# Kernel tuning notes

Measured on AMD Instinct MI355X. Metric: run time of the kernel, lower is better.

The kernel has to match this reference:

```python
import jax, jax.numpy as jnp
import numpy as np

E, H2, V = 128, 512, 50000  # embedding_size, hidden_size*2, output_size
H4 = 2 * H2


def _gru_cell(x, h, W_ih, W_hh, b_ih, b_hh):
    # PyTorch GRU cell: gates ordered (r, z, n)
    gi = x @ W_ih.T + b_ih
    gh = h @ W_hh.T + b_hh
    i_r, i_z, i_n = jnp.split(gi, 3, axis=-1)
    h_r, h_z, h_n = jnp.split(gh, 3, axis=-1)
    r = jax.nn.sigmoid(i_r + h_r)
    z = jax.nn.sigmoid(i_z + h_z)
    n = jnp.tanh(i_n + r * h_n)
    return (1.0 - z) * n + z * h


def setup_inputs() -> dict:
    key = jax.random.key(0)
    ks = jax.random.split(key, 24)
    B, T = 64, 400
    s = 0.02
    inp = {
        "input_ids": jax.random.randint(ks[0], (B, 1), 0, V),
        "pre_hidden": jax.random.normal(ks[1], (2, B, H2), jnp.float32),
        "encoder_outputs": jax.random.normal(ks[2], (B, T, H2), jnp.float32),
        "source_input": jax.random.randint(ks[3], (B, T), 0, V),
        "coverage_vector": jax.random.uniform(ks[4], (B, 1, T), jnp.float32),
        "emb_table": jax.random.normal(ks[5], (V, E), jnp.float32) * s,
        "W_ih0": jax.random.normal(ks[6], (3 * H2, E), jnp.float32) * s,
        "W_hh0": jax.random.normal(ks[7], (3 * H2, H2), jnp.float32) * s,
        "b_ih0": jnp.zeros((3 * H2,), jnp.float32),
        "b_hh0": jnp.zeros((3 * H2,), jnp.float32),
        "W_ih1": jax.random.normal(ks[8], (3 * H2, H2), jnp.float32) * s,
        "W_hh1": jax.random.normal(ks[9], (3 * H2, H2), jnp.float32) * s,
        "b_ih1": jnp.zeros((3 * H2,), jnp.float32),
        "b_hh1": jnp.zeros((3 * H2,), jnp.float32),
        "align_W": jax.random.normal(ks[10], (1, 3 * H2), jnp.float32) * s,
        "align_b": jnp.zeros((1,), jnp.float32),
        "cov_W": jax.random.normal(ks[11], (H2, 1), jnp.float32) * s,
        "cov_b": jnp.zeros((H2,), jnp.float32),
        "fc1_W": jax.random.normal(ks[12], (H4, H4), jnp.float32) * s,
        "fc1_b": jnp.zeros((H4,), jnp.float32),
        "fc2_W": jax.random.normal(ks[13], (V, H4), jnp.float32) * s,
        "fc2_b": jnp.zeros((V,), jnp.float32),
        "gen_W": jax.random.normal(ks[14], (1, H4 + E), jnp.float32) * s,
        "gen_b": jnp.zeros((1,), jnp.float32),
    }
    return inp


def reference(input_ids, pre_hidden, encoder_outputs, source_input, coverage_vector,
              emb_table, W_ih0, W_hh0, b_ih0, b_hh0, W_ih1, W_hh1, b_ih1, b_hh1,
              align_W, align_b, cov_W, cov_b, fc1_W, fc1_b, fc2_W, fc2_b, gen_W, gen_b):
    B, T = source_input.shape
    # embedding lookup (dropout omitted / eval mode)
    emb = emb_table[input_ids[:, 0]]                          # [B,E]
    # 2-layer GRU, single decode step
    h0 = _gru_cell(emb, pre_hidden[0], W_ih0, W_hh0, b_ih0, b_hh0)
    h1 = _gru_cell(h0, pre_hidden[1], W_ih1, W_hh1, b_ih1, b_hh1)
    current_hidden = jnp.stack([h0, h1], axis=0)              # [2,B,H2]
    s = h1                                                    # [B,H2]
    cov = coverage_vector[:, 0, :]                            # [B,T]
    # coverage projection: Linear(1 -> H2)
    cov_feat = cov[:, :, None] * cov_W[:, 0][None, None, :] + cov_b  # [B,T,H2]
    s_rep = jnp.broadcast_to(s[:, None, :], (B, T, s.shape[-1]))
    combine = jnp.concatenate([encoder_outputs, s_rep, cov_feat], axis=-1)  # [B,T,3*H2]
    scores = jnp.einsum('bti,i->bt', combine, align_W[0]) + align_b[0]
    attn = jax.nn.softmax(jnp.tanh(scores), axis=1)           # [B,T]
    # coverage loss: sum of elementwise min(attn, coverage)
    coverage_loss = jnp.sum(jnp.minimum(attn, cov))
    new_coverage = coverage_vector + attn[:, None, :]         # [B,1,T]
    context = jnp.einsum('bt,bth->bh', attn, encoder_outputs) # [B,H2]
    ni = jnp.tanh(jnp.concatenate([s, context], axis=-1) @ fc1_W.T + fc1_b)
    logits = ni @ fc2_W.T + fc2_b                             # [B,V]
    Pvocab = jax.nn.softmax(logits, axis=1)
    # vectorized copy distribution: scatter-add attention mass onto source token ids
    batch_idx = jnp.arange(B)[:, None]
    copy_prob = jnp.zeros((B, logits.shape[1]), logits.dtype).at[batch_idx, source_input].add(attn)
    gen_in = jnp.concatenate([context, s, emb], axis=-1)      # [B,H4+E]
    p_gen = jax.nn.sigmoid(gen_in @ gen_W.T + gen_b)          # [B,1]
    out = Pvocab * p_gen + copy_prob * (1.0 - p_gen)
    return (out, current_hidden, attn[:, None, :], copy_prob, new_coverage, coverage_loss)
```

## Files before the change

### kernel.cpp

```cpp
#include <hip/hip_runtime.h>
#include <hip/hip_bf16.h>
#include <cstddef>

#define BB 64
#define TT 400
#define EE 128
#define HH 512
#define H4 1024
#define VV 50000
#define NCH 8
#define LSTR 136

#define OFF_OUT     0
#define OFF_CURHID  (BB*VV)
#define OFF_ATTN    (OFF_CURHID + 2*BB*HH)
#define OFF_COPY    (OFF_ATTN + BB*TT)
#define OFF_NEWCOV  (OFF_COPY + BB*VV)
#define OFF_LOSS    (OFF_NEWCOV + BB*TT)

#define WS_S      0
#define WS_TS     (WS_S + BB*HH)
#define WS_ATTN   (WS_TS + BB*TT)
#define WS_NIB    (WS_ATTN + BB*TT)
#define WS_A1     (WS_NIB + BB*H4/2)
#define WS_AX0    (WS_A1 + BB*H4/2)
#define WS_AH0    (WS_AX0 + BB*EE/2)
#define WS_AH1    (WS_AH0 + BB*HH/2)
#define WS_AX1    (WS_AH1 + BB*HH/2)
#define WS_PGEN   (WS_AX1 + BB*HH/2)
#define WS_RM     (WS_PGEN + 64)
#define WS_RS     (WS_RM + 64)
#define WS_CTXP   (WS_RS + 64)
#define WS_LOGITS (WS_CTXP + BB*NCH*HH)

typedef __attribute__((ext_vector_type(8))) short short8v;
typedef __attribute__((ext_vector_type(4))) short short4v;
typedef __attribute__((ext_vector_type(4))) float f32x4;

__device__ __forceinline__ float wredsum(float v) {
#pragma unroll
  for (int o = 32; o > 0; o >>= 1) v += __shfl_down(v, o, 64);
  return v;
}
__device__ __forceinline__ float wredmax(float v) {
#pragma unroll
  for (int o = 32; o > 0; o >>= 1) v = fmaxf(v, __shfl_down(v, o, 64));
  return v;
}
__device__ __forceinline__ float dot4(float4 a, float4 b) {
  return a.x*b.x + a.y*b.y + a.z*b.z + a.w*b.w;
}
__device__ __forceinline__ float sigmoidf(float x) { return 1.f / (1.f + expf(-x)); }
__device__ __forceinline__ short bfh(float f) {
  union { __hip_bfloat16 h; short s; } u; u.h = __float2bfloat16(f); return u.s;
}
__device__ __forceinline__ float bf2f(short s) {
  union { unsigned int u; float f; } v; v.u = ((unsigned int)(unsigned short)s) << 16; return v.f;
}

__global__ void zero_prep_kernel(float* __restrict__ p, float* __restrict__ loss,
                                 float* __restrict__ rs,
                                 const float* __restrict__ embt, const int* __restrict__ ids,
                                 const float* __restrict__ preh,
                                 short* __restrict__ ax0, short* __restrict__ ah0,
                                 short* __restrict__ ah1) {
  int i = blockIdx.x * 256 + threadIdx.x;
  ((float4*)p)[i] = make_float4(0.f, 0.f, 0.f, 0.f);
  if (i == 0) loss[0] = 0.f;
  if (i < 64) rs[i] = 0.f;
  if (i < BB * EE) {
    int b = i >> 7, k = i & 127;
    ax0[i] = bfh(embt[(size_t)ids[b] * EE + k]);
  } else if (i < BB * EE + 2 * BB * HH) {
    int j = i - BB * EE;
    if (j < BB * HH) ah0[j] = bfh(preh[j]);
    else ah1[j - BB * HH] = bfh(preh[j]);
  }
}

template<int KX>
__global__ __launch_bounds__(384) void gru_mfma_kernel(
    const short* __restrict__ Ax, const short* __restrict__ Ah,
    const float* __restrict__ W_ih, const float* __restrict__ W_hh,
    const float* __restrict__ b_ih, const float* __restrict__ b_hh,
    const float* __restrict__ hprev,
    float* __restrict__ hout_f, float* __restrict__ hout_o,
    short* __restrict__ hout_b, int bstride) {
  __shared__ float P[2][3][16][16];
  const int w = threadIdx.x >> 6;
  const int lane = threadIdx.x & 63;
  const int r16 = lane & 15, kg = lane >> 4;
  const int j0 = (blockIdx.x & 31) * 16;
  const int bg = blockIdx.x >> 5;
  const int part = (w >= 3) ? 1 : 0;
  const int g = w - part * 3;
  const int K = part ? HH : KX;
  const float* Wm = part ? W_hh : W_ih;
  const short* Am = part ? Ah : Ax;

  f32x4 acc = {0.f, 0.f, 0.f, 0.f};
  const float* wp = Wm + (size_t)(g * HH + j0 + r16) * K + kg * 8;
  const short* ap = Am + (size_t)(bg * 16 + r16) * K + kg * 8;
#pragma unroll 4
  for (int k0 = 0; k0 < K; k0 += 32) {
    float4 w0 = *(const float4*)(wp + k0);
    float4 w1 = *(const float4*)(wp + k0 + 4);
    short8v a = *(const short8v*)(ap + k0);
    short8v bf;
    bf[0] = bfh(w0.x); bf[1] = bfh(w0.y); bf[2] = bfh(w0.z); bf[3] = bfh(w0.w);
    bf[4] = bfh(w1.x); bf[5] = bfh(w1.y); bf[6] = bfh(w1.z); bf[7] = bfh(w1.w);
    acc = __builtin_amdgcn_mfma_f32_16x16x32_bf16(a, bf, acc, 0, 0, 0);
  }
#pragma unroll
  for (int r = 0; r < 4; r++) P[part][g][kg * 4 + r][r16] = acc[r];
  __syncthreads();
  if (w == 0) {
    int col = j0 + r16;
    float bir = b_ih[col] + b_hh[col];
    float biz = b_ih[HH + col] + b_hh[HH + col];
    float bin = b_ih[2 * HH + col], bhn = b_hh[2 * HH + col];
#pragma unroll
    for (int r = 0; r < 4; r++) {
      int m = kg * 4 + r;
      int row = bg * 16 + m;
      float rv = sigmoidf(P[0][0][m][r16] + P[1][0][m][r16] + bir);
      float zv = sigmoidf(P[0][1][m][r16] + P[1][1][m][r16] + biz);
      float nv = tanhf(P[0][2][m][r16] + bin + rv * (P[1][2][m][r16] + bhn));
      float h = (1.f - zv) * nv + zv * hprev[(size_t)row * HH + col];
      hout_f[(size_t)row * HH + col] = h;
      hout_o[(size_t)row * HH + col] = h;
      hout_b[(size_t)row * bstride + col] = bfh(h);
    }
  }
}

__global__ void scores_kernel(const float* __restrict__ enc, const float* __restrict__ cov,
                              const float* __restrict__ aW, const float* __restrict__ ab,
                              const float* __restrict__ covW, const float* __restrict__ covb,
                              const float* __restrict__ s, float* __restrict__ ts) {
  int b = blockIdx.y;
  int wid = threadIdx.x >> 6, lane = threadIdx.x & 63;
  int t = blockIdx.x * 4 + wid;
  int i8 = lane * 8;
  const float* e = enc + ((size_t)b * TT + t) * HH + i8;
  float4 a0 = *(const float4*)&aW[i8],        a1 = *(const float4*)&aW[i8 + 4];
  float4 b0 = *(const float4*)&aW[HH + i8],   b1 = *(const float4*)&aW[HH + i8 + 4];
  float4 c0 = *(const float4*)&aW[2*HH + i8], c1 = *(const float4*)&aW[2*HH + i8 + 4];
  float4 s0 = *(const float4*)&s[(size_t)b * HH + i8], s1 = *(const float4*)&s[(size_t)b * HH + i8 + 4];
  float4 w0 = *(const float4*)&covW[i8],      w1 = *(const float4*)&covW[i8 + 4];
  float4 v0 = *(const float4*)&covb[i8],      v1 = *(const float4*)&covb[i8 + 4];
  float covbt = cov[b * TT + t];
  float p1 = dot4(*(const float4*)&e[0], a0) + dot4(*(const float4*)&e[4], a1)
           + dot4(s0, b0) + dot4(s1, b1)
           + dot4(v0, c0) + dot4(v1, c1);
  float p2 = dot4(w0, c0) + dot4(w1, c1);
  float d = wredsum(p1 + covbt * p2);
  if (lane == 0) ts[b * TT + t] = tanhf(d + ab[0]);
}

__global__ void attn_kernel(const float* __restrict__ ts, const float* __restrict__ cov,
                            const int* __restrict__ src,
                            float* __restrict__ wattn, float* __restrict__ dout,
                            float* __restrict__ outc) {
  int b = blockIdx.x, tid = threadIdx.x;
  int lane = tid & 63, wid = tid >> 6;
  __shared__ float sred[8];
  __shared__ float bval[2];
  float v = (tid < TT) ? ts[b * TT + tid] : -1e30f;
  float wm = wredmax(v);
  if (lane == 0) sred[wid] = wm;
  __syncthreads();
  if (wid == 0) {
    float r = (lane < 8) ? sred[lane] : -1e30f;
    r = wredmax(r);
    if (lane == 0) bval[0] = r;
  }
  __syncthreads();
  float m = bval[0];
  float e = (tid < TT) ? expf(v - m) : 0.f;
  float wsm = wredsum(e);
  __syncthreads();
  if (lane == 0) sred[wid] = wsm;
  __syncthreads();
  if (wid == 0) {
    float r = (lane < 8) ? sred[lane] : 0.f;
    r = wredsum(r);
    if (lane == 0) bval[1] = r;
  }
  __syncthreads();
  float denom = bval[1];
  float a = e / denom;
  float lp = 0.f;
  if (tid < TT) {
    wattn[b * TT + tid] = a;
    dout[OFF_ATTN + b * TT + tid] = a;
    float c = cov[b * TT + tid];
    dout[OFF_NEWCOV + b * TT + tid] = c + a;
    lp = fminf(a, c);
    atomicAdd(&outc[(size_t)b * VV + src[b * TT + tid]], a);
  }
  float wl = wredsum(lp);
  __syncthreads();
  if (lane == 0) sred[wid] = wl;
  __syncthreads();
  if (wid == 0) {
    float r = (lane < 8) ? sred[lane] : 0.f;
    r = wredsum(r);
    if (lane == 0) atomicAdd(&dout[OFF_LOSS], r);
  }
}

__global__ void ctx_part_kernel(const float* __restrict__ enc, const float* __restrict__ attn,
                                float* __restrict__ ctxp) {
  int b = blockIdx.x, c = blockIdx.y;
  int h = threadIdx.x;
  __shared__ float as[TT / NCH];
  if (h < TT / NCH) as[h] = attn[b * TT + c * (TT / NCH) + h];
  __syncthreads();
  const float* e = enc + ((size_t)b * TT + c * (TT / NCH)) * HH + h;
  float acc = 0.f;
#pragma unroll 10
  for (int t = 0; t < TT / NCH; t++) acc += as[t] * e[(size_t)t * HH];
  ctxp[((size_t)b * NCH + c) * HH + h] = acc;
}

__global__ void ctxred_pgen_kernel(const float* __restrict__ ctxp, const float* __restrict__ s,
                                   const float* __restrict__ embt, const int* __restrict__ ids,
                                   const float* __restrict__ gW, const float* __restrict__ gb,
                                   short* __restrict__ a1, float* __restrict__ pgen) {
  int b = blockIdx.x, tid = threadIdx.x;
  int lane = tid & 63, wid = tid >> 6;
  __shared__ float sred[8];
  float acc = 0.f;
#pragma unroll
  for (int c = 0; c < NCH; c++) acc += ctxp[((size_t)b * NCH + c) * HH + tid];
  a1[(size_t)b * H4 + HH + tid] = bfh(acc);
  float part = acc * gW[tid] + s[b * HH + tid] * gW[HH + tid];
  if (tid < EE) part += embt[(size_t)ids[b] * EE + tid] * gW[2 * HH + tid];
  float w = wredsum(part);
  if (lane == 0) sred[wid] = w;
  __syncthreads();
  if (wid == 0) {
    float r = (lane < 8) ? sred[lane] : 0.f;
    r = wredsum(r);
    if (lane == 0) pgen[b] = sigmoidf(r + gb[0]);
  }
}

__global__ __launch_bounds__(256) void fc1_kernel(const short* __restrict__ a1,
                                                  const float* __restrict__ W,
                                                  const float* __restrict__ bias,
                                                  short* __restrict__ nib) {
  __shared__ float part[4096];
  const int w = threadIdx.x >> 6;
  const int lane = threadIdx.x & 63;
  const int r16 = lane & 15, kg = lane >> 4;
  const int v0 = blockIdx.x * 16;
  const int kb = w * 256;

  f32x4 acc0 = {0.f,0.f,0.f,0.f}, acc1 = {0.f,0.f,0.f,0.f};
  f32x4 acc2 = {0.f,0.f,0.f,0.f}, acc3 = {0.f,0.f,0.f,0.f};
  const float* wp = W + (size_t)(v0 + r16) * H4 + kb + kg * 8;
  const short* ap = a1 + (size_t)r16 * H4 + kb + kg * 8;
#pragma unroll 4
  for (int k0 = 0; k0 < 256; k0 += 32) {
    float4 w0 = *(const float4*)(wp + k0);
    float4 w1 = *(const float4*)(wp + k0 + 4);
    short8v a0 = *(const short8v*)(ap + k0);
    short8v a1v = *(const short8v*)(ap + 16 * H4 + k0);
    short8v a2 = *(const short8v*)(ap + 32 * H4 + k0);
    short8v a3 = *(const short8v*)(ap + 48 * H4 + k0);
    short8v bf;
    bf[0] = bfh(w0.x); bf[1] = bfh(w0.y); bf[2] = bfh(w0.z); bf[3] = bfh(w0.w);
    bf[4] = bfh(w1.x); bf[5] = bfh(w1.y); bf[6] = bfh(w1.z); bf[7] = bfh(w1.w);
    acc0 = __builtin_amdgcn_mfma_f32_16x16x32_bf16(a0, bf, acc0, 0, 0, 0);
    acc1 = __builtin_amdgcn_mfma_f32_16x16x32_bf16(a1v, bf, acc1, 0, 0, 0);
    acc2 = __builtin_amdgcn_mfma_f32_16x16x32_bf16(a2, bf, acc2, 0, 0, 0);
    acc3 = __builtin_amdgcn_mfma_f32_16x16x32_bf16(a3, bf, acc3, 0, 0, 0);
  }
  float* pb = part + w * 1024;
#pragma unroll
  for (int r = 0; r < 4; r++) {
    pb[(kg * 4 + r) * 16 + r16]      = acc0[r];
    pb[(16 + kg * 4 + r) * 16 + r16] = acc1[r];
    pb[(32 + kg * 4 + r) * 16 + r16] = acc2[r];
    pb[(48 + kg * 4 + r) * 16 + r16] = acc3[r];
  }
  __syncthreads();
  int idx = threadIdx.x * 4;
  int m = idx >> 4, c0 = idx & 15;
  f32x4 s0 = *(const f32x4*)(part + idx);
  f32x4 s1 = *(const f32x4*)(part + 1024 + idx);
  f32x4 s2 = *(const f32x4*)(part + 2048 + idx);
  f32x4 s3 = *(const f32x4*)(part + 3072 + idx);
  f32x4 bv = *(const f32x4*)(bias + v0 + c0);
  f32x4 o = s0 + s1 + s2 + s3 + bv;
#pragma unroll
  for (int j = 0; j < 4; j++)
    nib[(size_t)m * H4 + v0 + c0 + j] = bfh(tanhf(o[j]));
}

__global__ __launch_bounds__(256) void fc2_kernel(const short* __restrict__ nib,
                                                  const float* __restrict__ W,
                                                  const float* __restrict__ bias,
                                                  short* __restrict__ logits_bf,
                                                  float* __restrict__ rs) {
  __shared__ short Wl[64 * LSTR];
  __shared__ short Al[64 * LSTR];
  const int tid = threadIdx.x;
  const int w = tid >> 6, lane = tid & 63;
  const int r16 = lane & 15, kg = lane >> 4;
  const int v0 = blockIdx.x * 64;
  const int srow = tid >> 2, quad = tid & 3;
  const int vr = min(v0 + srow, VV - 1);

  f32x4 acc[4];
#pragma unroll
  for (int i = 0; i < 4; i++) acc[i] = (f32x4){0.f, 0.f, 0.f, 0.f};

  const float* wsrc = W + (size_t)vr * H4 + quad * 4;
  const short* asrc = nib + (size_t)srow * H4 + quad * 8;

  float4 wreg[8];
  short8v areg[4];
#pragma unroll
  for (int j = 0; j < 8; j++) wreg[j] = *(const float4*)(wsrc + j * 16);
#pragma unroll
  for (int j = 0; j < 4; j++) areg[j] = *(const short8v*)(asrc + j * 32);

  for (int ks = 0; ks < 8; ks++) {
    {
      char* dst = (char*)Wl + srow * (LSTR * 2) + quad * 8;
#pragma unroll
      for (int j = 0; j < 8; j++) {
        float4 f = wreg[j];
        short4v h; h[0] = bfh(f.x); h[1] = bfh(f.y); h[2] = bfh(f.z); h[3] = bfh(f.w);
        *(short4v*)(dst + j * 32) = h;
      }
      char* adst = (char*)Al + srow * (LSTR * 2) + quad * 16;
#pragma unroll
      for (int j = 0; j < 4; j++)
        *(short8v*)(adst + j * 64) = areg[j];
    }
    __syncthreads();
    if (ks < 7) {
      const float* ws2 = wsrc + (ks + 1) * 128;
      const short* as2 = asrc + (ks + 1) * 128;
#pragma unroll
      for (int j = 0; j < 8; j++) wreg[j] = *(const float4*)(ws2 + j * 16);
#pragma unroll
      for (int j = 0; j < 4; j++) areg[j] = *(const short8v*)(as2 + j * 32);
    }
#pragma unroll
    for (int s = 0; s < 4; s++) {
      short8v wf = *(const short8v*)((char*)Wl + (w * 16 + r16) * (LSTR * 2) + s * 64 + kg * 16);
#pragma unroll
      for (int i = 0; i < 4; i++) {
        short8v af = *(const short8v*)((char*)Al + (i * 16 + r16) * (LSTR * 2) + s * 64 + kg * 16);
        acc[i] = __builtin_amdgcn_mfma_f32_16x16x32_bf16(af, wf, acc[i], 0, 0, 0);
      }
    }
    __syncthreads();
  }

  float* sc = (float*)Wl;
#pragma unroll
  for (int i = 0; i < 4; i++)
#pragma unroll
    for (int r = 0; r < 4; r++)
      sc[(i * 16 + kg * 4 + r) * 64 + w * 16 + r16] = acc[i][r];
  __syncthreads();
  int m = tid >> 2, q = tid & 3;
  int colbase = v0 + q * 16;
  float esum = 0.f;
  if (colbase < VV) {
    const float* scp = sc + m * 64 + q * 16;
    short8v lo, hi;
#pragma unroll
    for (int j = 0; j < 8; j++) {
      short lb = bfh(scp[j] + bias[colbase + j]);
      lo[j] = lb;
      esum += expf(bf2f(lb));
    }
#pragma unroll
    for (int j = 0; j < 8; j++) {
      short lb = bfh(scp[8 + j] + bias[colbase + 8 + j]);
      hi[j] = lb;
      esum += expf(bf2f(lb));
    }
    *(short8v*)(logits_bf + (size_t)m * VV + colbase)     = lo;
    *(short8v*)(logits_bf + (size_t)m * VV + colbase + 8) = hi;
  }
  esum += __shfl_down(esum, 2, 4);
  esum += __shfl_down(esum, 1, 4);
  if (q == 0) atomicAdd(&rs[m], esum);
}

__global__ void final_kernel(const short* __restrict__ logits_bf, const float* __restrict__ rs,
                             const float* __restrict__ pgen,
                             const float* __restrict__ copy, float* __restrict__ out) {
  int i = blockIdx.x * 256 + threadIdx.x;
  int b = (i * 4) / VV;
  float p = pgen[b], s = rs[b];
  short4v l = ((const short4v*)logits_bf)[i];
  float4 c = ((const float4*)copy)[i];
  float q = 1.f - p;
  float ps = p / s;
  float4 o;
  o.x = expf(bf2f(l[0])) * ps + c.x * q;
  o.y = expf(bf2f(l[1])) * ps + c.y * q;
  o.z = expf(bf2f(l[2])) * ps + c.z * q;
  o.w = expf(bf2f(l[3])) * ps + c.w * q;
  ((float4*)out)[i] = o;
}

extern "C" void kernel_launch(void* const* d_in, const int* in_sizes, int n_in,
                              void* d_out, int out_size, void* d_ws, size_t ws_size,
                              hipStream_t stream) {
  const int*   ids  = (const int*)d_in[0];
  const float* preh = (const float*)d_in[1];
  const float* enc  = (const float*)d_in[2];
  const int*   src  = (const int*)d_in[3];
  const float* cov  = (const float*)d_in[4];
  const float* embt = (const float*)d_in[5];
  const float* Wih0 = (const float*)d_in[6];
  const float* Whh0 = (const float*)d_in[7];
  const float* bih0 = (const float*)d_in[8];
  const float* bhh0 = (const float*)d_in[9];
  const float* Wih1 = (const float*)d_in[10];
  const float* Whh1 = (const float*)d_in[11];
  const float* bih1 = (const float*)d_in[12];
  const float* bhh1 = (const float*)d_in[13];
  const float* aW   = (const float*)d_in[14];
  const float* ab   = (const float*)d_in[15];
  const float* covW = (const float*)d_in[16];
  const float* covb = (const float*)d_in[17];
  const float* f1W  = (const float*)d_in[18];
  const float* f1b  = (const float*)d_in[19];
  const float* f2W  = (const float*)d_in[20];
  const float* f2b  = (const float*)d_in[21];
  const float* gW   = (const float*)d_in[22];
  const float* gb   = (const float*)d_in[23];
  float* out = (float*)d_out;
  float* ws  = (float*)d_ws;

  zero_prep_kernel<<<3125, 256, 0, stream>>>(out + OFF_COPY, out + OFF_LOSS, ws + WS_RS,
                                             embt, ids, preh,
                                             (short*)(ws + WS_AX0), (short*)(ws + WS_AH0),
                                             (short*)(ws + WS_AH1));
  gru_mfma_kernel<EE><<<128, 384, 0, stream>>>(
      (const short*)(ws + WS_AX0), (const short*)(ws + WS_AH0),
      Wih0, Whh0, bih0, bhh0, preh,
      out + OFF_CURHID, out + OFF_CURHID, (short*)(ws + WS_AX1), HH);
  gru_mfma_kernel<HH><<<128, 384, 0, stream>>>(
      (const short*)(ws + WS_AX1), (const short*)(ws + WS_AH1),
      Wih1, Whh1, bih1, bhh1, preh + BB * HH,
      ws + WS_S, out + OFF_CURHID + BB * HH, (short*)(ws + WS_A1), H4);
  scores_kernel<<<dim3(100, 64), 256, 0, stream>>>(enc, cov, aW, ab, covW, covb,
                                                   ws + WS_S, ws + WS_TS);
  attn_kernel<<<64, 512, 0, stream>>>(ws + WS_TS, cov, src, ws + WS_ATTN, out,
                                      out + OFF_COPY);
  ctx_part_kernel<<<dim3(64, NCH), 512, 0, stream>>>(enc, ws + WS_ATTN, ws + WS_CTXP);
  ctxred_pgen_kernel<<<64, 512, 0, stream>>>(ws + WS_CTXP, ws + WS_S, embt, ids, gW, gb,
                                             (short*)(ws + WS_A1), ws + WS_PGEN);
  fc1_kernel<<<64, 256, 0, stream>>>((const short*)(ws + WS_A1), f1W, f1b,
                                     (short*)(ws + WS_NIB));
  fc2_kernel<<<782, 256, 0, stream>>>((const short*)(ws + WS_NIB), f2W, f2b,
                                      (short*)(ws + WS_LOGITS), ws + WS_RS);
  final_kernel<<<3125, 256, 0, stream>>>((const short*)(ws + WS_LOGITS), ws + WS_RS,
                                         ws + WS_PGEN, out + OFF_COPY, out);
}
```

Baseline: 130.2 us.

## Merge dependent kernel launches using software grid barriers

```diff
diff --git a/kernel.cpp b/kernel.cpp
--- a/kernel.cpp
+++ b/kernel.cpp
@@ -30,7 +30,8 @@
 #define WS_PGEN   (WS_AX1 + BB*HH/2)
 #define WS_RM     (WS_PGEN + 64)
 #define WS_RS     (WS_RM + 64)
-#define WS_CTXP   (WS_RS + 64)
+#define WS_BAR    (WS_RS + 64)
+#define WS_CTXP   (WS_BAR + 8)
 #define WS_LOGITS (WS_CTXP + BB*NCH*HH)
 
 typedef __attribute__((ext_vector_type(8))) short short8v;
@@ -58,8 +59,19 @@
   union { unsigned int u; float f; } v; v.u = ((unsigned int)(unsigned short)s) << 16; return v.f;
 }
 
+__device__ __forceinline__ void grid_barrier(unsigned int* bar, unsigned int target) {
+  __syncthreads();
+  if (threadIdx.x == 0) {
+    __hip_atomic_fetch_add(bar, 1u, __ATOMIC_ACQ_REL, __HIP_MEMORY_SCOPE_AGENT);
+    while (__hip_atomic_load(bar, __ATOMIC_ACQUIRE, __HIP_MEMORY_SCOPE_AGENT) < target) {
+      __builtin_amdgcn_s_sleep(2);
+    }
+  }
+  __syncthreads();
+}
+
 __global__ void zero_prep_kernel(float* __restrict__ p, float* __restrict__ loss,
-                                 float* __restrict__ rs,
+                                 float* __restrict__ rs, unsigned int* __restrict__ bar,
                                  const float* __restrict__ embt, const int* __restrict__ ids,
                                  const float* __restrict__ preh,
                                  short* __restrict__ ax0, short* __restrict__ ah0,
@@ -68,6 +80,7 @@
   ((float4*)p)[i] = make_float4(0.f, 0.f, 0.f, 0.f);
   if (i == 0) loss[0] = 0.f;
   if (i < 64) rs[i] = 0.f;
+  if (i < 8) bar[i] = 0u;
   if (i < BB * EE) {
     int b = i >> 7, k = i & 127;
     ax0[i] = bfh(embt[(size_t)ids[b] * EE + k]);
@@ -78,15 +91,13 @@
   }
 }
 
-template<int KX>
-__global__ __launch_bounds__(384) void gru_mfma_kernel(
+__device__ __forceinline__ void gru_layer(
     const short* __restrict__ Ax, const short* __restrict__ Ah,
     const float* __restrict__ W_ih, const float* __restrict__ W_hh,
     const float* __restrict__ b_ih, const float* __restrict__ b_hh,
     const float* __restrict__ hprev,
     float* __restrict__ hout_f, float* __restrict__ hout_o,
-    short* __restrict__ hout_b, int bstride) {
-  __shared__ float P[2][3][16][16];
+    short* __restrict__ hout_b, int bstride, int KX, float* __restrict__ Pf) {
   const int w = threadIdx.x >> 6;
   const int lane = threadIdx.x & 63;
   const int r16 = lane & 15, kg = lane >> 4;
@@ -112,7 +123,8 @@
     acc = __builtin_amdgcn_mfma_f32_16x16x32_bf16(a, bf, acc, 0, 0, 0);
   }
 #pragma unroll
-  for (int r = 0; r < 4; r++) P[part][g][kg * 4 + r][r16] = acc[r];
+  for (int r = 0; r < 4; r++)
+    Pf[((part * 3 + g) * 16 + (kg * 4 + r)) * 16 + r16] = acc[r];
   __syncthreads();
   if (w == 0) {
     int col = j0 + r16;
@@ -123,15 +135,33 @@
     for (int r = 0; r < 4; r++) {
       int m = kg * 4 + r;
       int row = bg * 16 + m;
-      float rv = sigmoidf(P[0][0][m][r16] + P[1][0][m][r16] + bir);
-      float zv = sigmoidf(P[0][1][m][r16] + P[1][1][m][r16] + biz);
-      float nv = tanhf(P[0][2][m][r16] + bin + rv * (P[1][2][m][r16] + bhn));
+      float rv = sigmoidf(Pf[(0 * 16 + m) * 16 + r16] + Pf[(3 * 16 + m) * 16 + r16] + bir);
+      float zv = sigmoidf(Pf[(1 * 16 + m) * 16 + r16] + Pf[(4 * 16 + m) * 16 + r16] + biz);
+      float nv = tanhf(Pf[(2 * 16 + m) * 16 + r16] + bin +
+                       rv * (Pf[(5 * 16 + m) * 16 + r16] + bhn));
       float h = (1.f - zv) * nv + zv * hprev[(size_t)row * HH + col];
       hout_f[(size_t)row * HH + col] = h;
       hout_o[(size_t)row * HH + col] = h;
       hout_b[(size_t)row * bstride + col] = bfh(h);
     }
   }
+}
+
+__global__ __launch_bounds__(384) void gru01_kernel(
+    const short* __restrict__ ax0, const short* __restrict__ ah0, const short* __restrict__ ah1,
+    const float* __restrict__ Wih0, const float* __restrict__ Whh0,
+    const float* __restrict__ bih0, const float* __restrict__ bhh0,
+    const float* __restrict__ Wih1, const float* __restrict__ Whh1,
+    const float* __restrict__ bih1, const float* __restrict__ bhh1,
+    const float* __restrict__ preh, float* __restrict__ curhid,
+    float* __restrict__ s_f32, short* __restrict__ ax1, short* __restrict__ a1,
+    unsigned int* __restrict__ bar) {
+  __shared__ float Pf[2 * 3 * 16 * 16];
+  gru_layer(ax0, ah0, Wih0, Whh0, bih0, bhh0, preh,
+            curhid, curhid, ax1, HH, EE, Pf);
+  grid_barrier(bar, 128);
+  gru_layer(ax1, ah1, Wih1, Whh1, bih1, bhh1, preh + BB * HH,
+            s_f32, curhid + BB * HH, a1, H4, HH, Pf);
 }
 
 __global__ void scores_kernel(const float* __restrict__ enc, const float* __restrict__ cov,
@@ -210,101 +240,100 @@
   }
 }
 
-__global__ void ctx_part_kernel(const float* __restrict__ enc, const float* __restrict__ attn,
-                                float* __restrict__ ctxp) {
-  int b = blockIdx.x, c = blockIdx.y;
-  int h = threadIdx.x;
-  __shared__ float as[TT / NCH];
-  if (h < TT / NCH) as[h] = attn[b * TT + c * (TT / NCH) + h];
-  __syncthreads();
-  const float* e = enc + ((size_t)b * TT + c * (TT / NCH)) * HH + h;
-  float acc = 0.f;
+__global__ __launch_bounds__(512, 4) void ctxfc1_kernel(
+    const float* __restrict__ enc, const float* __restrict__ attn,
+    const float* __restrict__ s, const float* __restrict__ embt,
+    const int* __restrict__ ids, const float* __restrict__ gW,
+    const float* __restrict__ gb, const float* __restrict__ f1W,
+    const float* __restrict__ f1b,
+    float* __restrict__ ctxp, short* __restrict__ a1, float* __restrict__ pgen,
+    short* __restrict__ nib, unsigned int* __restrict__ bar) {
+  __shared__ float shm[8192];
+  const int tid = threadIdx.x;
+
+  {
+    int b = blockIdx.x >> 3, c = blockIdx.x & 7;
+    if (tid < TT / NCH) shm[tid] = attn[b * TT + c * (TT / NCH) + tid];
+    __syncthreads();
+    const float* e = enc + ((size_t)b * TT + c * (TT / NCH)) * HH + tid;
+    float acc = 0.f;
 #pragma unroll 10
-  for (int t = 0; t < TT / NCH; t++) acc += as[t] * e[(size_t)t * HH];
-  ctxp[((size_t)b * NCH + c) * HH + h] = acc;
-}
-
-__global__ void ctxred_pgen_kernel(const float* __restrict__ ctxp, const float* __restrict__ s,
-                                   const float* __restrict__ embt, const int* __restrict__ ids,
-                                   const float* __restrict__ gW, const float* __restrict__ gb,
-                                   short* __restrict__ a1, float* __restrict__ pgen) {
-  int b = blockIdx.x, tid = threadIdx.x;
-  int lane = tid & 63, wid = tid >> 6;
-  __shared__ float sred[8];
-  float acc = 0.f;
-#pragma unroll
-  for (int c = 0; c < NCH; c++) acc += ctxp[((size_t)b * NCH + c) * HH + tid];
-  a1[(size_t)b * H4 + HH + tid] = bfh(acc);
-  float part = acc * gW[tid] + s[b * HH + tid] * gW[HH + tid];
-  if (tid < EE) part += embt[(size_t)ids[b] * EE + tid] * gW[2 * HH + tid];
-  float w = wredsum(part);
-  if (lane == 0) sred[wid] = w;
-  __syncthreads();
-  if (wid == 0) {
-    float r = (lane < 8) ? sred[lane] : 0.f;
-    r = wredsum(r);
-    if (lane == 0) pgen[b] = sigmoidf(r + gb[0]);
-  }
-}
-
-__global__ __launch_bounds__(256) void fc1_kernel(const short* __restrict__ a1,
-                                                  const float* __restrict__ W,
-                                                  const float* __restrict__ bias,
-                                                  short* __restrict__ nib) {
-  __shared__ float part[4096];
-  const int w = threadIdx.x >> 6;
-  const int lane = threadIdx.x & 63;
-  const int r16 = lane & 15, kg = lane >> 4;
-  const int v0 = blockIdx.x * 16;
-  const int kb = w * 256;
-
-  f32x4 acc0 = {0.f,0.f,0.f,0.f}, acc1 = {0.f,0.f,0.f,0.f};
-  f32x4 acc2 = {0.f,0.f,0.f,0.f}, acc3 = {0.f,0.f,0.f,0.f};
-  const float* wp = W + (size_t)(v0 + r16) * H4 + kb + kg * 8;
-  const short* ap = a1 + (size_t)r16 * H4 + kb + kg * 8;
-#pragma unroll 4
-  for (int k0 = 0; k0 < 256; k0 += 32) {
-    float4 w0 = *(const float4*)(wp + k0);
-    float4 w1 = *(const float4*)(wp + k0 + 4);
-    short8v a0 = *(const short8v*)(ap + k0);
-    short8v a1v = *(const short8v*)(ap + 16 * H4 + k0);
-    short8v a2 = *(const short8v*)(ap + 32 * H4 + k0);
-    short8v a3 = *(const short8v*)(ap + 48 * H4 + k0);
-    short8v bf;
-    bf[0] = bfh(w0.x); bf[1] = bfh(w0.y); bf[2] = bfh(w0.z); bf[3] = bfh(w0.w);
-    bf[4] = bfh(w1.x); bf[5] = bfh(w1.y); bf[6] = bfh(w1.z); bf[7] = bfh(w1.w);
-    acc0 = __builtin_amdgcn_mfma_f32_16x16x32_bf16(a0, bf, acc0, 0, 0, 0);
-    acc1 = __builtin_amdgcn_mfma_f32_16x16x32_bf16(a1v, bf, acc1, 0, 0, 0);
-    acc2 = __builtin_amdgcn_mfma_f32_16x16x32_bf16(a2, bf, acc2, 0, 0, 0);
-    acc3 = __builtin_amdgcn_mfma_f32_16x16x32_bf16(a3, bf, acc3, 0, 0, 0);
-  }
-  float* pb = part + w * 1024;
-#pragma unroll
-  for (int r = 0; r < 4; r++) {
-    pb[(kg * 4 + r) * 16 + r16]      = acc0[r];
-    pb[(16 + kg * 4 + r) * 16 + r16] = acc1[r];
-    pb[(32 + kg * 4 + r) * 16 + r16] = acc2[r];
-    pb[(48 + kg * 4 + r) * 16 + r16] = acc3[r];
-  }
-  __syncthreads();
-  int idx = threadIdx.x * 4;
-  int m = idx >> 4, c0 = idx & 15;
-  f32x4 s0 = *(const f32x4*)(part + idx);
-  f32x4 s1 = *(const f32x4*)(part + 1024 + idx);
-  f32x4 s2 = *(const f32x4*)(part + 2048 + idx);
-  f32x4 s3 = *(const f32x4*)(part + 3072 + idx);
-  f32x4 bv = *(const f32x4*)(bias + v0 + c0);
-  f32x4 o = s0 + s1 + s2 + s3 + bv;
-#pragma unroll
-  for (int j = 0; j < 4; j++)
-    nib[(size_t)m * H4 + v0 + c0 + j] = bfh(tanhf(o[j]));
-}
-
-__global__ __launch_bounds__(256) void fc2_kernel(const short* __restrict__ nib,
-                                                  const float* __restrict__ W,
-                                                  const float* __restrict__ bias,
-                                                  short* __restrict__ logits_bf,
-                                                  float* __restrict__ rs) {
+    for (int t = 0; t < TT / NCH; t++) acc += shm[t] * e[(size_t)t * HH];
+    ctxp[((size_t)b * NCH + c) * HH + tid] = acc;
+  }
+  grid_barrier(bar + 0, 512);
+
+  if (blockIdx.x < 64) {
+    int b = blockIdx.x;
+    int lane = tid & 63, wid = tid >> 6;
+    float acc = 0.f;
+#pragma unroll
+    for (int c = 0; c < NCH; c++) acc += ctxp[((size_t)b * NCH + c) * HH + tid];
+    a1[(size_t)b * H4 + HH + tid] = bfh(acc);
+    float part = acc * gW[tid] + s[b * HH + tid] * gW[HH + tid];
+    if (tid < EE) part += embt[(size_t)ids[b] * EE + tid] * gW[2 * HH + tid];
+    float w = wredsum(part);
+    if (lane == 0) shm[wid] = w;
+    __syncthreads();
+    if (wid == 0) {
+      float r = (lane < 8) ? shm[lane] : 0.f;
+      r = wredsum(r);
+      if (lane == 0) pgen[b] = sigmoidf(r + gb[0]);
+    }
+  }
+  grid_barrier(bar + 1, 512);
+  if (blockIdx.x >= 64) return;
+
+  {
+    const int w = tid >> 6, lane = tid & 63;
+    const int r16 = lane & 15, kg = lane >> 4;
+    const int v0 = blockIdx.x * 16;
+    const int kb = w * 128;
+    f32x4 acc0 = {0.f,0.f,0.f,0.f}, acc1 = {0.f,0.f,0.f,0.f};
+    f32x4 acc2 = {0.f,0.f,0.f,0.f}, acc3 = {0.f,0.f,0.f,0.f};
+    const float* wp = f1W + (size_t)(v0 + r16) * H4 + kb + kg * 8;
+    const short* ap = a1 + (size_t)r16 * H4 + kb + kg * 8;
+#pragma unroll
+    for (int k0 = 0; k0 < 128; k0 += 32) {
+      float4 w0 = *(const float4*)(wp + k0);
+      float4 w1 = *(const float4*)(wp + k0 + 4);
+      short8v a0 = *(const short8v*)(ap + k0);
+      short8v a1v = *(const short8v*)(ap + 16 * H4 + k0);
+      short8v a2 = *(const short8v*)(ap + 32 * H4 + k0);
+      short8v a3 = *(const short8v*)(ap + 48 * H4 + k0);
+      short8v bf;
+      bf[0] = bfh(w0.x); bf[1] = bfh(w0.y); bf[2] = bfh(w0.z); bf[3] = bfh(w0.w);
+      bf[4] = bfh(w1.x); bf[5] = bfh(w1.y); bf[6] = bfh(w1.z); bf[7] = bfh(w1.w);
+      acc0 = __builtin_amdgcn_mfma_f32_16x16x32_bf16(a0, bf, acc0, 0, 0, 0);
+      acc1 = __builtin_amdgcn_mfma_f32_16x16x32_bf16(a1v, bf, acc1, 0, 0, 0);
+      acc2 = __builtin_amdgcn_mfma_f32_16x16x32_bf16(a2, bf, acc2, 0, 0, 0);
+      acc3 = __builtin_amdgcn_mfma_f32_16x16x32_bf16(a3, bf, acc3, 0, 0, 0);
+    }
+    float* pb = shm + w * 1024;
+#pragma unroll
+    for (int r = 0; r < 4; r++) {
+      pb[(kg * 4 + r) * 16 + r16]      = acc0[r];
+      pb[(16 + kg * 4 + r) * 16 + r16] = acc1[r];
+      pb[(32 + kg * 4 + r) * 16 + r16] = acc2[r];
+      pb[(48 + kg * 4 + r) * 16 + r16] = acc3[r];
+    }
+    __syncthreads();
+    int idx = tid * 2;
+    int m = idx >> 4, c0 = idx & 15;
+    float s0 = 0.f, s1 = 0.f;
+#pragma unroll
+    for (int p = 0; p < 8; p++) { s0 += shm[p * 1024 + idx]; s1 += shm[p * 1024 + idx + 1]; }
+    nib[(size_t)m * H4 + v0 + c0]     = bfh(tanhf(s0 + f1b[v0 + c0]));
+    nib[(size_t)m * H4 + v0 + c0 + 1] = bfh(tanhf(s1 + f1b[v0 + c0 + 1]));
+  }
+}
+
+__global__ __launch_bounds__(256, 4) void fc2final_kernel(
+    const short* __restrict__ nib, const float* __restrict__ W,
+    const float* __restrict__ bias, short* __restrict__ logits_bf,
+    float* __restrict__ rs, const float* __restrict__ pgen,
+    const float* __restrict__ copy, float* __restrict__ out,
+    unsigned int* __restrict__ bar) {
   __shared__ short Wl[64 * LSTR];
   __shared__ short Al[64 * LSTR];
   const int tid = threadIdx.x;
@@ -394,24 +423,22 @@
   esum += __shfl_down(esum, 2, 4);
   esum += __shfl_down(esum, 1, 4);
   if (q == 0) atomicAdd(&rs[m], esum);
-}
-
-__global__ void final_kernel(const short* __restrict__ logits_bf, const float* __restrict__ rs,
-                             const float* __restrict__ pgen,
-                             const float* __restrict__ copy, float* __restrict__ out) {
-  int i = blockIdx.x * 256 + threadIdx.x;
-  int b = (i * 4) / VV;
-  float p = pgen[b], s = rs[b];
-  short4v l = ((const short4v*)logits_bf)[i];
-  float4 c = ((const float4*)copy)[i];
-  float q = 1.f - p;
-  float ps = p / s;
-  float4 o;
-  o.x = expf(bf2f(l[0])) * ps + c.x * q;
-  o.y = expf(bf2f(l[1])) * ps + c.y * q;
-  o.z = expf(bf2f(l[2])) * ps + c.z * q;
-  o.w = expf(bf2f(l[3])) * ps + c.w * q;
-  ((float4*)out)[i] = o;
+
+  grid_barrier(bar, 782);
+  for (int i = blockIdx.x * 256 + tid; i < BB * VV / 4; i += 782 * 256) {
+    int b = (i * 4) / VV;
+    float p = pgen[b], sden = rs[b];
+    short4v l = ((const short4v*)logits_bf)[i];
+    float4 c = ((const float4*)copy)[i];
+    float qg = 1.f - p;
+    float ps = p / sden;
+    float4 o;
+    o.x = expf(bf2f(l[0])) * ps + c.x * qg;
+    o.y = expf(bf2f(l[1])) * ps + c.y * qg;
+    o.z = expf(bf2f(l[2])) * ps + c.z * qg;
+    o.w = expf(bf2f(l[3])) * ps + c.w * qg;
+    ((float4*)out)[i] = o;
+  }
 }
 
 extern "C" void kernel_launch(void* const* d_in, const int* in_sizes, int n_in,
@@ -443,30 +470,26 @@
   const float* gb   = (const float*)d_in[23];
   float* out = (float*)d_out;
   float* ws  = (float*)d_ws;
+  unsigned int* bar = (unsigned int*)(ws + WS_BAR);
 
   zero_prep_kernel<<<3125, 256, 0, stream>>>(out + OFF_COPY, out + OFF_LOSS, ws + WS_RS,
-                                             embt, ids, preh,
+                                             bar, embt, ids, preh,
                                              (short*)(ws + WS_AX0), (short*)(ws + WS_AH0),
                                              (short*)(ws + WS_AH1));
-  gru_mfma_kernel<EE><<<128, 384, 0, stream>>>(
-      (const short*)(ws + WS_AX0), (const short*)(ws + WS_AH0),
-      Wih0, Whh0, bih0, bhh0, preh,
-      out + OFF_CURHID, out + OFF_CURHID, (short*)(ws + WS_AX1), HH);
-  gru_mfma_kernel<HH><<<128, 384, 0, stream>>>(
-      (const short*)(ws + WS_AX1), (const short*)(ws + WS_AH1),
-      Wih1, Whh1, bih1, bhh1, preh + BB * HH,
-      ws + WS_S, out + OFF_CURHID + BB * HH, (short*)(ws + WS_A1), H4);
+  gru01_kernel<<<128, 384, 0, stream>>>(
+      (const short*)(ws + WS_AX0), (const short*)(ws + WS_AH0), (const short*)(ws + WS_AH1),
+      Wih0, Whh0, bih0, bhh0, Wih1, Whh1, bih1, bhh1,
+      preh, out + OFF_CURHID, ws + WS_S,
+      (short*)(ws + WS_AX1), (short*)(ws + WS_A1), bar + 0);
   scores_kernel<<<dim3(100, 64), 256, 0, stream>>>(enc, cov, aW, ab, covW, covb,
                                                    ws + WS_S, ws + WS_TS);
   attn_kernel<<<64, 512, 0, stream>>>(ws + WS_TS, cov, src, ws + WS_ATTN, out,
                                       out + OFF_COPY);
-  ctx_part_kernel<<<dim3(64, NCH), 512, 0, stream>>>(enc, ws + WS_ATTN, ws + WS_CTXP);
-  ctxred_pgen_kernel<<<64, 512, 0, stream>>>(ws + WS_CTXP, ws + WS_S, embt, ids, gW, gb,
-                                             (short*)(ws + WS_A1), ws + WS_PGEN);
-  fc1_kernel<<<64, 256, 0, stream>>>((const short*)(ws + WS_A1), f1W, f1b,
-                                     (short*)(ws + WS_NIB));
-  fc2_kernel<<<782, 256, 0, stream>>>((const short*)(ws + WS_NIB), f2W, f2b,
-                                      (short*)(ws + WS_LOGITS), ws + WS_RS);
-  final_kernel<<<3125, 256, 0, stream>>>((const short*)(ws + WS_LOGITS), ws + WS_RS,
-                                         ws + WS_PGEN, out + OFF_COPY, out);
-}
+  ctxfc1_kernel<<<512, 512, 0, stream>>>(enc, ws + WS_ATTN, ws + WS_S, embt, ids, gW, gb,
+                                         f1W, f1b, ws + WS_CTXP,
+                                         (short*)(ws + WS_A1), ws + WS_PGEN,
+                                         (short*)(ws + WS_NIB), bar + 1);
+  fc2final_kernel<<<782, 256, 0, stream>>>((const short*)(ws + WS_NIB), f2W, f2b,
+                                           (short*)(ws + WS_LOGITS), ws + WS_RS,
+                                           ws + WS_PGEN, out + OFF_COPY, out, bar + 3);
+}
```

After: 348.4 us. 168% more time.

## Fuse two GRU layer kernels into one launch with a grid barrier

Applied to the files above, without the earlier changes.

```diff
diff --git a/kernel.cpp b/kernel.cpp
--- a/kernel.cpp
+++ b/kernel.cpp
@@ -30,7 +30,8 @@
 #define WS_PGEN   (WS_AX1 + BB*HH/2)
 #define WS_RM     (WS_PGEN + 64)
 #define WS_RS     (WS_RM + 64)
-#define WS_CTXP   (WS_RS + 64)
+#define WS_BAR    (WS_RS + 64)
+#define WS_CTXP   (WS_BAR + 8)
 #define WS_LOGITS (WS_CTXP + BB*NCH*HH)
 
 typedef __attribute__((ext_vector_type(8))) short short8v;
@@ -58,8 +59,19 @@
   union { unsigned int u; float f; } v; v.u = ((unsigned int)(unsigned short)s) << 16; return v.f;
 }
 
+__device__ __forceinline__ void grid_barrier(unsigned int* bar, unsigned int target) {
+  __syncthreads();
+  if (threadIdx.x == 0) {
+    __hip_atomic_fetch_add(bar, 1u, __ATOMIC_ACQ_REL, __HIP_MEMORY_SCOPE_AGENT);
+    while (__hip_atomic_load(bar, __ATOMIC_ACQUIRE, __HIP_MEMORY_SCOPE_AGENT) < target) {
+      __builtin_amdgcn_s_sleep(8);
+    }
+  }
+  __syncthreads();
+}
+
 __global__ void zero_prep_kernel(float* __restrict__ p, float* __restrict__ loss,
-                                 float* __restrict__ rs,
+                                 float* __restrict__ rs, unsigned int* __restrict__ bar,
                                  const float* __restrict__ embt, const int* __restrict__ ids,
                                  const float* __restrict__ preh,
                                  short* __restrict__ ax0, short* __restrict__ ah0,
@@ -68,6 +80,7 @@
   ((float4*)p)[i] = make_float4(0.f, 0.f, 0.f, 0.f);
   if (i == 0) loss[0] = 0.f;
   if (i < 64) rs[i] = 0.f;
+  if (i < 8) bar[i] = 0u;
   if (i < BB * EE) {
     int b = i >> 7, k = i & 127;
     ax0[i] = bfh(embt[(size_t)ids[b] * EE + k]);
@@ -78,15 +91,13 @@
   }
 }
 
-template<int KX>
-__global__ __launch_bounds__(384) void gru_mfma_kernel(
+__device__ __forceinline__ void gru_layer(
     const short* __restrict__ Ax, const short* __restrict__ Ah,
     const float* __restrict__ W_ih, const float* __restrict__ W_hh,
     const float* __restrict__ b_ih, const float* __restrict__ b_hh,
     const float* __restrict__ hprev,
     float* __restrict__ hout_f, float* __restrict__ hout_o,
-    short* __restrict__ hout_b, int bstride) {
-  __shared__ float P[2][3][16][16];
+    short* __restrict__ hout_b, int bstride, int KX, float* __restrict__ Pf) {
   const int w = threadIdx.x >> 6;
   const int lane = threadIdx.x & 63;
   const int r16 = lane & 15, kg = lane >> 4;
@@ -112,7 +123,8 @@
     acc = __builtin_amdgcn_mfma_f32_16x16x32_bf16(a, bf, acc, 0, 0, 0);
   }
 #pragma unroll
-  for (int r = 0; r < 4; r++) P[part][g][kg * 4 + r][r16] = acc[r];
+  for (int r = 0; r < 4; r++)
+    Pf[((part * 3 + g) * 16 + (kg * 4 + r)) * 16 + r16] = acc[r];
   __syncthreads();
   if (w == 0) {
     int col = j0 + r16;
@@ -123,15 +135,33 @@
     for (int r = 0; r < 4; r++) {
       int m = kg * 4 + r;
       int row = bg * 16 + m;
-      float rv = sigmoidf(P[0][0][m][r16] + P[1][0][m][r16] + bir);
-      float zv = sigmoidf(P[0][1][m][r16] + P[1][1][m][r16] + biz);
-      float nv = tanhf(P[0][2][m][r16] + bin + rv * (P[1][2][m][r16] + bhn));
+      float rv = sigmoidf(Pf[(0 * 16 + m) * 16 + r16] + Pf[(3 * 16 + m) * 16 + r16] + bir);
+      float zv = sigmoidf(Pf[(1 * 16 + m) * 16 + r16] + Pf[(4 * 16 + m) * 16 + r16] + biz);
+      float nv = tanhf(Pf[(2 * 16 + m) * 16 + r16] + bin +
+                       rv * (Pf[(5 * 16 + m) * 16 + r16] + bhn));
       float h = (1.f - zv) * nv + zv * hprev[(size_t)row * HH + col];
       hout_f[(size_t)row * HH + col] = h;
       hout_o[(size_t)row * HH + col] = h;
       hout_b[(size_t)row * bstride + col] = bfh(h);
     }
   }
+}
+
+__global__ __launch_bounds__(384) void gru01_kernel(
+    const short* __restrict__ ax0, const short* __restrict__ ah0, const short* __restrict__ ah1,
+    const float* __restrict__ Wih0, const float* __restrict__ Whh0,
+    const float* __restrict__ bih0, const float* __restrict__ bhh0,
+    const float* __restrict__ Wih1, const float* __restrict__ Whh1,
+    const float* __restrict__ bih1, const float* __restrict__ bhh1,
+    const float* __restrict__ preh, float* __restrict__ curhid,
+    float* __restrict__ s_f32, short* __restrict__ ax1, short* __restrict__ a1,
+    unsigned int* __restrict__ bar) {
+  __shared__ float Pf[2 * 3 * 16 * 16];
+  gru_layer(ax0, ah0, Wih0, Whh0, bih0, bhh0, preh,
+            curhid, curhid, ax1, HH, EE, Pf);
+  grid_barrier(bar, 128);
+  gru_layer(ax1, ah1, Wih1, Whh1, bih1, bhh1, preh + BB * HH,
+            s_f32, curhid + BB * HH, a1, H4, HH, Pf);
 }
 
 __global__ void scores_kernel(const float* __restrict__ enc, const float* __restrict__ cov,
@@ -443,19 +473,17 @@
   const float* gb   = (const float*)d_in[23];
   float* out = (float*)d_out;
   float* ws  = (float*)d_ws;
+  unsigned int* bar = (unsigned int*)(ws + WS_BAR);
 
   zero_prep_kernel<<<3125, 256, 0, stream>>>(out + OFF_COPY, out + OFF_LOSS, ws + WS_RS,
-                                             embt, ids, preh,
+                                             bar, embt, ids, preh,
                                              (short*)(ws + WS_AX0), (short*)(ws + WS_AH0),
                                              (short*)(ws + WS_AH1));
-  gru_mfma_kernel<EE><<<128, 384, 0, stream>>>(
-      (const short*)(ws + WS_AX0), (const short*)(ws + WS_AH0),
-      Wih0, Whh0, bih0, bhh0, preh,
-      out + OFF_CURHID, out + OFF_CURHID, (short*)(ws + WS_AX1), HH);
-  gru_mfma_kernel<HH><<<128, 384, 0, stream>>>(
-      (const short*)(ws + WS_AX1), (const short*)(ws + WS_AH1),
-      Wih1, Whh1, bih1, bhh1, preh + BB * HH,
-      ws + WS_S, out + OFF_CURHID + BB * HH, (short*)(ws + WS_A1), H4);
+  gru01_kernel<<<128, 384, 0, stream>>>(
+      (const short*)(ws + WS_AX0), (const short*)(ws + WS_AH0), (const short*)(ws + WS_AH1),
+      Wih0, Whh0, bih0, bhh0, Wih1, Whh1, bih1, bhh1,
+      preh, out + OFF_CURHID, ws + WS_S,
+      (short*)(ws + WS_AX1), (short*)(ws + WS_A1), bar + 0);
   scores_kernel<<<dim3(100, 64), 256, 0, stream>>>(enc, cov, aW, ab, covW, covb,
                                                    ws + WS_S, ws + WS_TS);
   attn_kernel<<<64, 512, 0, stream>>>(ws + WS_TS, cov, src, ws + WS_ATTN, out,
```

Result: slower. 136.6 us (+4.9%).
